# Optimization experiments

Measured on AMD Instinct MI355X. Metric: run time of the kernel, lower is better.

## Reference

```python
import jax, jax.numpy as jnp
import numpy as np

N = 100000   # node_num
E = 1000000  # edges per relation
DIN, DH, DOUT = 64, 32, 64  # in_dim, out_dim//2, out_dim
EPS = 1e-5


def setup_inputs() -> dict:
    key = jax.random.key(0)
    ks = jax.random.split(key, 32)
    def w(k, shape):
        fan_in = shape[0]
        return jax.random.normal(k, shape, dtype=jnp.float32) / np.sqrt(fan_in)
    inp = {}
    inp["init_emb"] = jax.random.normal(ks[0], (N, DIN), dtype=jnp.float32)
    inp["pos_edges"] = jax.random.randint(ks[1], (2, E), 0, N, dtype=jnp.int32)
    inp["neg_edges"] = jax.random.randint(ks[2], (2, E), 0, N, dtype=jnp.int32)
    # conv1: two relation layers + self-loop layer, 64 -> 32
    inp["c1_Wp"] = w(ks[3], (DIN, DH)); inp["c1_bp"] = jnp.zeros((DH,), jnp.float32)
    inp["c1_Wn"] = w(ks[4], (DIN, DH)); inp["c1_bn"] = jnp.zeros((DH,), jnp.float32)
    inp["c1_Ws"] = w(ks[5], (DIN, DH)); inp["c1_bs"] = jnp.zeros((DH,), jnp.float32)
    # conv2: 32 -> 32
    inp["c2_Wp"] = w(ks[6], (DH, DH)); inp["c2_bp"] = jnp.zeros((DH,), jnp.float32)
    inp["c2_Wn"] = w(ks[7], (DH, DH)); inp["c2_bn"] = jnp.zeros((DH,), jnp.float32)
    inp["c2_Ws"] = w(ks[8], (DH, DH)); inp["c2_bs"] = jnp.zeros((DH,), jnp.float32)
    # self.weight: Linear(32 -> 64)
    inp["w_W"] = w(ks[9], (DH, DOUT)); inp["w_b"] = jnp.zeros((DOUT,), jnp.float32)
    # readout MLP: Linear(64,64)+BN+ReLU, Linear(64,64)+BN+ReLU, Linear(64,1)
    inp["m1_W"] = w(ks[10], (DOUT, DOUT)); inp["m1_b"] = jnp.zeros((DOUT,), jnp.float32)
    inp["g1"] = jnp.ones((DOUT,), jnp.float32); inp["b1"] = jnp.zeros((DOUT,), jnp.float32)
    inp["m2_W"] = w(ks[11], (DOUT, DOUT)); inp["m2_b"] = jnp.zeros((DOUT,), jnp.float32)
    inp["g2"] = jnp.ones((DOUT,), jnp.float32); inp["b2"] = jnp.zeros((DOUT,), jnp.float32)
    inp["m3_W"] = w(ks[12], (DOUT, 1)); inp["m3_b"] = jnp.zeros((1,), jnp.float32)
    return inp


def _conv(x, pe, ne, Wp, bp, Wn, bn_, Ws, bs):
    # gather -> per-relation linear -> scatter_add, summed over 2 relations + self loop
    mp = x[pe[0]] @ Wp + bp                                  # [E, d_out]
    agg = jax.ops.segment_sum(mp, pe[1], num_segments=N)      # [N, d_out]
    mn = x[ne[0]] @ Wn + bn_
    agg = agg + jax.ops.segment_sum(mn, ne[1], num_segments=N)
    return agg + x @ Ws + bs


def _batchnorm(h, g, b):
    m = h.mean(axis=0)
    v = h.var(axis=0)
    return (h - m) * jax.lax.rsqrt(v + EPS) * g + b


def reference(init_emb, pos_edges, neg_edges,
              c1_Wp, c1_bp, c1_Wn, c1_bn, c1_Ws, c1_bs,
              c2_Wp, c2_bp, c2_Wn, c2_bn, c2_Ws, c2_bs,
              w_W, w_b, m1_W, m1_b, g1, b1, m2_W, m2_b, g2, b2, m3_W, m3_b):
    z = jnp.tanh(_conv(init_emb, pos_edges, neg_edges, c1_Wp, c1_bp, c1_Wn, c1_bn, c1_Ws, c1_bs))
    z = jnp.tanh(_conv(z, pos_edges, neg_edges, c2_Wp, c2_bp, c2_Wn, c2_bn, c2_Ws, c2_bs))
    z = jnp.tanh(z @ w_W + w_b)                               # [N, 64]
    h = jax.nn.relu(_batchnorm(z @ m1_W + m1_b, g1, b1))      # dropout p=0.2 disabled (eval)
    h = jax.nn.relu(_batchnorm(h @ m2_W + m2_b, g2, b2))
    prob = jax.nn.sigmoid(h @ m3_W + m3_b)                    # [N, 1]
    return (z, prob)
```

## Files before the change

kernel.cpp:

```cpp
#include <hip/hip_runtime.h>
#include <cstdint>
#include <cstddef>

#define NN 100000
#define EE 1000000
#define EPSF 1e-5f
#define NBUK 391
#define NBUK2 (2*NBUK)
#define NBLK 256
#define EPB 7813
#define GSB 782
#define GTILES ((NN + 63) / 64)
#define MLP_GRID 512
#define XFT (NN / 16)
#define XF_GRID 512

typedef __attribute__((ext_vector_type(8))) short bf16x8;
typedef __attribute__((ext_vector_type(4))) float f32x4;

__device__ __forceinline__ void fatomic(float* p, float v) { unsafeAtomicAdd(p, v); }

__device__ __forceinline__ short f2bf(float f) {
    unsigned u = __float_as_uint(f);
    u += 0x7FFF + ((u >> 16) & 1);
    return (short)(u >> 16);
}
__device__ __forceinline__ float bf2f(short s) {
    return __uint_as_float(((unsigned)(unsigned short)s) << 16);
}
__device__ __forceinline__ void split8(const float4 v0, const float4 v1, bf16x8& hi, bf16x8& lo) {
    float a[8] = {v0.x, v0.y, v0.z, v0.w, v1.x, v1.y, v1.z, v1.w};
    #pragma unroll
    for (int i = 0; i < 8; i++) {
        short h = f2bf(a[i]);
        hi[i] = h;
        lo[i] = f2bf(a[i] - bf2f(h));
    }
}
__device__ __forceinline__ int kmap(int kg, int i) {
    return (i < 4) ? kg * 4 + i : 16 + kg * 4 + (i - 4);
}

__device__ __forceinline__ void edge_of(const int* __restrict__ pe, const int* __restrict__ ne,
                                        int s, int& src, int& dst, int& bucket) {
    if (s < EE) { src = pe[s]; dst = pe[EE + s]; bucket = dst >> 8; }
    else        { src = ne[s - EE]; dst = ne[s]; bucket = NBUK + (dst >> 8); }
}

__global__ __launch_bounds__(256) void k_hist(const int* __restrict__ pe,
                                              const int* __restrict__ ne,
                                              int* __restrict__ hist) {
    __shared__ int lh[NBUK2];
    for (int i = threadIdx.x; i < NBUK2; i += 256) lh[i] = 0;
    __syncthreads();
    int start = blockIdx.x * EPB, end = min(start + EPB, 2 * EE);
    for (int s = start + threadIdx.x; s < end; s += 256) {
        int src, dst, bucket;
        edge_of(pe, ne, s, src, dst, bucket);
        atomicAdd(&lh[bucket], 1);
    }
    __syncthreads();
    for (int i = threadIdx.x; i < NBUK2; i += 256)
        hist[i * NBLK + blockIdx.x] = lh[i];
}

__global__ __launch_bounds__(256) void k_gscan1(const int* __restrict__ in,
                                                int* __restrict__ out,
                                                int* __restrict__ partials) {
    int i = blockIdx.x * 256 + threadIdx.x;
    int v = in[i];
    __shared__ int s[256];
    s[threadIdx.x] = v;
    __syncthreads();
    for (int off = 1; off < 256; off <<= 1) {
        int u = (threadIdx.x >= off) ? s[threadIdx.x - off] : 0;
        __syncthreads();
        s[threadIdx.x] += u;
        __syncthreads();
    }
    out[i] = s[threadIdx.x] - v;
    if (threadIdx.x == 255) partials[blockIdx.x] = s[255];
}

__global__ __launch_bounds__(1024) void k_gscan2(int* __restrict__ partials) {
    __shared__ int s[1024];
    int v = (threadIdx.x < GSB) ? partials[threadIdx.x] : 0;
    s[threadIdx.x] = v;
    __syncthreads();
    for (int off = 1; off < 1024; off <<= 1) {
        int u = (threadIdx.x >= off) ? s[threadIdx.x - off] : 0;
        __syncthreads();
        s[threadIdx.x] += u;
        __syncthreads();
    }
    if (threadIdx.x < GSB) partials[threadIdx.x] = s[threadIdx.x] - v;
}

__global__ __launch_bounds__(256) void k_gscan3(const int* __restrict__ partials,
                                                int* __restrict__ out) {
    out[blockIdx.x * 256 + threadIdx.x] += partials[blockIdx.x];
}

__global__ __launch_bounds__(256) void k_binscatter(const int* __restrict__ pe,
                                                    const int* __restrict__ ne,
                                                    const int* __restrict__ soff,
                                                    unsigned* __restrict__ staging) {
    __shared__ int cur[NBUK2];
    for (int i = threadIdx.x; i < NBUK2; i += 256)
        cur[i] = soff[i * NBLK + blockIdx.x];
    __syncthreads();
    int start = blockIdx.x * EPB, end = min(start + EPB, 2 * EE);
    for (int s = start + threadIdx.x; s < end; s += 256) {
        int src, dst, bucket;
        edge_of(pe, ne, s, src, dst, bucket);
        int pos = atomicAdd(&cur[bucket], 1);
        staging[pos] = ((unsigned)(dst & 255) << 20) | (unsigned)src;
    }
}

__global__ __launch_bounds__(256) void k_local(const unsigned* __restrict__ staging,
                                               const int* __restrict__ soff,
                                               int* __restrict__ rpP,
                                               int* __restrict__ rpN,
                                               int* __restrict__ csrAll) {
    int bucket = blockIdx.x;
    int rel = bucket >= NBUK;
    int nodeBase = (bucket - rel * NBUK) << 8;
    int bstart = soff[bucket * NBLK];
    int bend = (bucket == NBUK2 - 1) ? 2 * EE : soff[(bucket + 1) * NBLK];
    int tid = threadIdx.x;
    __shared__ int deg[256], sc[256];
    deg[tid] = 0;
    __syncthreads();
    for (int i = bstart + tid; i < bend; i += 256) {
        int d = (int)(staging[i] >> 20);
        atomicAdd(&deg[d], 1);
    }
    __syncthreads();
    int dv = deg[tid];
    sc[tid] = dv;
    __syncthreads();
    for (int off = 1; off < 256; off <<= 1) {
        int u = (tid >= off) ? sc[tid - off] : 0;
        __syncthreads();
        sc[tid] += u;
        __syncthreads();
    }
    int lrp = sc[tid] - dv;
    int nCount = min(256, NN - nodeBase);
    int relbase = rel ? EE : 0;
    if (tid < nCount) (rel ? rpN : rpP)[nodeBase + tid] = bstart - relbase + lrp;
    if (bucket == NBUK - 1 && tid == 0) rpP[NN] = EE;
    if (bucket == NBUK2 - 1 && tid == 0) rpN[NN] = EE;
    deg[tid] = lrp;
    __syncthreads();
    for (int i = bstart + tid; i < bend; i += 256) {
        unsigned v = staging[i];
        int d = (int)(v >> 20);
        int src = (int)(v & 0xFFFFFu);
        int slot = atomicAdd(&deg[d], 1);
        csrAll[bstart + slot] = src;
    }
}

__global__ __launch_bounds__(192) __attribute__((amdgpu_waves_per_eu(2, 4)))
void k_xf1(const float* __restrict__ x,
           const float* __restrict__ Wp,
           const float* __restrict__ Wn,
           const float* __restrict__ Ws,
           float* __restrict__ xp,
           float* __restrict__ xn,
           float* __restrict__ xs) {
    int tid = threadIdx.x;
    int wvm = tid >> 6;
    int l = tid & 63;
    int r16 = l & 15, kg = l >> 4;
    const float* W = (wvm == 0) ? Wp : (wvm == 1) ? Wn : Ws;
    float* outm = (wvm == 0) ? xp : (wvm == 1) ? xn : xs;

    bf16x8 bh[2][2], bl[2][2];
    #pragma unroll
    for (int ct = 0; ct < 2; ct++)
        #pragma unroll
        for (int h = 0; h < 2; h++)
            #pragma unroll
            for (int i = 0; i < 8; i++) {
                int k = h * 32 + kmap(kg, i);
                float w = W[k * 32 + ct * 16 + r16];
                short hi = f2bf(w);
                bh[ct][h][i] = hi;
                bl[ct][h][i] = f2bf(w - bf2f(hi));
            }

    for (int tile = blockIdx.x; tile < XFT; tile += XF_GRID) {
        int rbase = tile * 16;
        int arow = rbase + r16;
        bf16x8 ah[2], al[2];
        #pragma unroll
        for (int h = 0; h < 2; h++) {
            int k0 = h * 32 + kg * 4;
            int k1 = h * 32 + 16 + kg * 4;
            float4 v0 = *(const float4*)&x[(size_t)arow * 64 + k0];
            float4 v1 = *(const float4*)&x[(size_t)arow * 64 + k1];
            split8(v0, v1, ah[h], al[h]);
        }
        f32x4 acc[2];
        #pragma unroll
        for (int ct = 0; ct < 2; ct++) { acc[ct][0] = 0.f; acc[ct][1] = 0.f; acc[ct][2] = 0.f; acc[ct][3] = 0.f; }
        #pragma unroll
        for (int h = 0; h < 2; h++)
            #pragma unroll
            for (int ct = 0; ct < 2; ct++) {
                acc[ct] = __builtin_amdgcn_mfma_f32_16x16x32_bf16(ah[h], bh[ct][h], acc[ct], 0, 0, 0);
                acc[ct] = __builtin_amdgcn_mfma_f32_16x16x32_bf16(al[h], bh[ct][h], acc[ct], 0, 0, 0);
                acc[ct] = __builtin_amdgcn_mfma_f32_16x16x32_bf16(ah[h], bl[ct][h], acc[ct], 0, 0, 0);
            }
        #pragma unroll
        for (int ct = 0; ct < 2; ct++)
            #pragma unroll
            for (int i = 0; i < 4; i++)
                outm[(size_t)(rbase + kg * 4 + i) * 32 + ct * 16 + r16] = acc[ct][i];
    }
}

__global__ __launch_bounds__(192) __attribute__((amdgpu_waves_per_eu(2, 4)))
void k_xf2(const float* __restrict__ z,
           const float* __restrict__ Wp,
           const float* __restrict__ Wn,
           const float* __restrict__ Ws,
           float* __restrict__ xp,
           float* __restrict__ xn,
           float* __restrict__ xs) {
    int tid = threadIdx.x;
    int wvm = tid >> 6;
    int l = tid & 63;
    int r16 = l & 15, kg = l >> 4;
    const float* W = (wvm == 0) ? Wp : (wvm == 1) ? Wn : Ws;
    float* outm = (wvm == 0) ? xp : (wvm == 1) ? xn : xs;

    bf16x8 bh[2], bl[2];
    #pragma unroll
    for (int ct = 0; ct < 2; ct++)
        #pragma unroll
        for (int i = 0; i < 8; i++) {
            int k = kmap(kg, i);
            float w = W[k * 32 + ct * 16 + r16];
            short hi = f2bf(w);
            bh[ct][i] = hi;
            bl[ct][i] = f2bf(w - bf2f(hi));
        }

    for (int tile = blockIdx.x; tile < XFT; tile += XF_GRID) {
        int rbase = tile * 16;
        int arow = rbase + r16;
        float4 v0 = *(const float4*)&z[(size_t)arow * 32 + kg * 4];
        float4 v1 = *(const float4*)&z[(size_t)arow * 32 + 16 + kg * 4];
        bf16x8 ah, al;
        split8(v0, v1, ah, al);
        f32x4 acc[2];
        #pragma unroll
        for (int ct = 0; ct < 2; ct++) { acc[ct][0] = 0.f; acc[ct][1] = 0.f; acc[ct][2] = 0.f; acc[ct][3] = 0.f; }
        #pragma unroll
        for (int ct = 0; ct < 2; ct++) {
            acc[ct] = __builtin_amdgcn_mfma_f32_16x16x32_bf16(ah, bh[ct], acc[ct], 0, 0, 0);
            acc[ct] = __builtin_amdgcn_mfma_f32_16x16x32_bf16(al, bh[ct], acc[ct], 0, 0, 0);
            acc[ct] = __builtin_amdgcn_mfma_f32_16x16x32_bf16(ah, bl[ct], acc[ct], 0, 0, 0);
        }
        #pragma unroll
        for (int ct = 0; ct < 2; ct++)
            #pragma unroll
            for (int i = 0; i < 4; i++)
                outm[(size_t)(rbase + kg * 4 + i) * 32 + ct * 16 + r16] = acc[ct][i];
    }
}

__device__ __forceinline__ float pull_rel(const float* __restrict__ xsrc,
                                          const int* __restrict__ csr,
                                          int b0, int b1, int j, float acc) {
    for (int base = b0; base < b1; base += 32) {
        int rem = b1 - base;
        int cnt = min(rem, 32);
        int idx = (j < rem) ? csr[base + j] : 0;
        int i = 0;
        for (; i + 4 <= cnt; i += 4) {
            int s0 = __shfl(idx, i, 32);
            int s1 = __shfl(idx, i + 1, 32);
            int s2 = __shfl(idx, i + 2, 32);
            int s3 = __shfl(idx, i + 3, 32);
            float v0 = xsrc[(size_t)s0 * 32 + j];
            float v1 = xsrc[(size_t)s1 * 32 + j];
            float v2 = xsrc[(size_t)s2 * 32 + j];
            float v3 = xsrc[(size_t)s3 * 32 + j];
            acc += v0; acc += v1; acc += v2; acc += v3;
        }
        for (; i < cnt; i++) {
            int s = __shfl(idx, i, 32);
            acc += xsrc[(size_t)s * 32 + j];
        }
    }
    return acc;
}

__global__ __launch_bounds__(256) void k_pull(const float* __restrict__ xp,
                                              const float* __restrict__ xn,
                                              const float* __restrict__ xs,
                                              const int* __restrict__ rpP,
                                              const int* __restrict__ csrP,
                                              const int* __restrict__ rpN,
                                              const int* __restrict__ csrN,
                                              const float* __restrict__ bp,
                                              const float* __restrict__ bn,
                                              const float* __restrict__ bs,
                                              float* __restrict__ out) {
    int j = threadIdx.x & 31;
    int hw = (blockIdx.x * 256 + threadIdx.x) >> 5;
    const int nhw = (2048 * 256) >> 5;
    float bpj = bp[j], bnj = bn[j], bsj = bs[j];
    for (int n = hw; n < NN; n += nhw) {
        int p0 = rpP[n], p1 = rpP[n + 1];
        int n0 = rpN[n], n1 = rpN[n + 1];
        float acc = xs[(size_t)n * 32 + j] + bsj
                  + (float)(p1 - p0) * bpj + (float)(n1 - n0) * bnj;
        acc = pull_rel(xp, csrP, p0, p1, j, acc);
        acc = pull_rel(xn, csrN, n0, n1, j, acc);
        out[(size_t)n * 32 + j] = tanhf(acc);
    }
}

__global__ __launch_bounds__(256) __attribute__((amdgpu_waves_per_eu(2, 4)))
void k_wlin(const float* __restrict__ z2,
            const float* __restrict__ Wl,
            const float* __restrict__ bl,
            float* __restrict__ z) {
    int tid = threadIdx.x;
    int wv = tid >> 6;
    int l = tid & 63;
    int r16 = l & 15, kg = l >> 4;

    bf16x8 bh[4], blo[4];
    #pragma unroll
    for (int ct = 0; ct < 4; ct++)
        #pragma unroll
        for (int i = 0; i < 8; i++) {
            int k = kmap(kg, i);
            float w = Wl[k * 64 + ct * 16 + r16];
            short hi = f2bf(w);
            bh[ct][i] = hi;
            blo[ct][i] = f2bf(w - bf2f(hi));
        }
    float bj[4];
    #pragma unroll
    for (int ct = 0; ct < 4; ct++) bj[ct] = bl[ct * 16 + r16];

    for (int tile = blockIdx.x * 4 + wv; tile < XFT; tile += XF_GRID * 4) {
        int rbase = tile * 16;
        int arow = rbase + r16;
        float4 v0 = *(const float4*)&z2[(size_t)arow * 32 + kg * 4];
        float4 v1 = *(const float4*)&z2[(size_t)arow * 32 + 16 + kg * 4];
        bf16x8 ah, al;
        split8(v0, v1, ah, al);
        f32x4 acc[4];
        #pragma unroll
        for (int ct = 0; ct < 4; ct++) { acc[ct][0] = 0.f; acc[ct][1] = 0.f; acc[ct][2] = 0.f; acc[ct][3] = 0.f; }
        #pragma unroll
        for (int ct = 0; ct < 4; ct++) {
            acc[ct] = __builtin_amdgcn_mfma_f32_16x16x32_bf16(ah, bh[ct], acc[ct], 0, 0, 0);
            acc[ct] = __builtin_amdgcn_mfma_f32_16x16x32_bf16(al, bh[ct], acc[ct], 0, 0, 0);
            acc[ct] = __builtin_amdgcn_mfma_f32_16x16x32_bf16(ah, blo[ct], acc[ct], 0, 0, 0);
        }
        #pragma unroll
        for (int ct = 0; ct < 4; ct++)
            #pragma unroll
            for (int i = 0; i < 4; i++)
                z[(size_t)(rbase + kg * 4 + i) * 64 + ct * 16 + r16] = tanhf(acc[ct][i] + bj[ct]);
    }
}

__global__ __launch_bounds__(256) __attribute__((amdgpu_waves_per_eu(2, 4)))
void k_mlp(const float* __restrict__ in,
           const float* __restrict__ a1,
           const float* __restrict__ c1,
           int doBN,
           const float* __restrict__ W,
           const float* __restrict__ b,
           float* __restrict__ out,
           float* __restrict__ colsum,
           float* __restrict__ colsq) {
    __shared__ float scol[64], ssq[64];
    int tid = threadIdx.x;
    if (tid < 64) { scol[tid] = 0.f; ssq[tid] = 0.f; }
    int wv = tid >> 6;
    int l = tid & 63;
    int r16 = l & 15, kg = l >> 4;

    bf16x8 bf[4][2];
    #pragma unroll
    for (int ct = 0; ct < 4; ct++)
        #pragma unroll
        for (int h = 0; h < 2; h++)
            #pragma unroll
            for (int i = 0; i < 8; i++) {
                int k = h * 32 + kmap(kg, i);
                bf[ct][h][i] = f2bf(W[k * 64 + ct * 16 + r16]);
            }
    float bj[4];
    #pragma unroll
    for (int ct = 0; ct < 4; ct++) bj[ct] = b[ct * 16 + r16];

    float av0[2][4], cv0[2][4], av1[2][4], cv1[2][4];
    #pragma unroll
    for (int h = 0; h < 2; h++) {
        int k0 = h * 32 + kg * 4;
        int k1 = h * 32 + 16 + kg * 4;
        #pragma unroll
        for (int i = 0; i < 4; i++) {
            av0[h][i] = doBN ? a1[k0 + i] : 1.f;
            cv0[h][i] = doBN ? c1[k0 + i] : 0.f;
            av1[h][i] = doBN ? a1[k1 + i] : 1.f;
            cv1[h][i] = doBN ? c1[k1 + i] : 0.f;
        }
    }

    float lsum[4] = {0.f, 0.f, 0.f, 0.f}, lsq[4] = {0.f, 0.f, 0.f, 0.f};

    for (int tile = blockIdx.x; tile < GTILES; tile += MLP_GRID) {
        int base = tile * 64;
        int arow = base + wv * 16 + r16;
        bool rv = arow < NN;
        bf16x8 af[2];
        #pragma unroll
        for (int h = 0; h < 2; h++) {
            int k0 = h * 32 + kg * 4;
            int k1 = h * 32 + 16 + kg * 4;
            float4 v0 = rv ? *(const float4*)&in[(size_t)arow * 64 + k0]
                           : make_float4(0.f, 0.f, 0.f, 0.f);
            float4 v1 = rv ? *(const float4*)&in[(size_t)arow * 64 + k1]
                           : make_float4(0.f, 0.f, 0.f, 0.f);
            if (doBN) {
                v0.x = fmaxf(v0.x * av0[h][0] + cv0[h][0], 0.f);
                v0.y = fmaxf(v0.y * av0[h][1] + cv0[h][1], 0.f);
                v0.z = fmaxf(v0.z * av0[h][2] + cv0[h][2], 0.f);
                v0.w = fmaxf(v0.w * av0[h][3] + cv0[h][3], 0.f);
                v1.x = fmaxf(v1.x * av1[h][0] + cv1[h][0], 0.f);
                v1.y = fmaxf(v1.y * av1[h][1] + cv1[h][1], 0.f);
                v1.z = fmaxf(v1.z * av1[h][2] + cv1[h][2], 0.f);
                v1.w = fmaxf(v1.w * av1[h][3] + cv1[h][3], 0.f);
            }
            af[h][0] = f2bf(v0.x); af[h][1] = f2bf(v0.y);
            af[h][2] = f2bf(v0.z); af[h][3] = f2bf(v0.w);
            af[h][4] = f2bf(v1.x); af[h][5] = f2bf(v1.y);
            af[h][6] = f2bf(v1.z); af[h][7] = f2bf(v1.w);
        }

        f32x4 acc[4];
        #pragma unroll
        for (int ct = 0; ct < 4; ct++) { acc[ct][0] = 0.f; acc[ct][1] = 0.f; acc[ct][2] = 0.f; acc[ct][3] = 0.f; }
        #pragma unroll
        for (int h = 0; h < 2; h++)
            #pragma unroll
            for (int ct = 0; ct < 4; ct++)
                acc[ct] = __builtin_amdgcn_mfma_f32_16x16x32_bf16(af[h], bf[ct][h], acc[ct], 0, 0, 0);

        #pragma unroll
        for (int ct = 0; ct < 4; ct++) {
            int col = ct * 16 + r16;
            #pragma unroll
            for (int i = 0; i < 4; i++) {
                int orow = base + wv * 16 + kg * 4 + i;
                if (orow < NN) {
                    float s = acc[ct][i] + bj[ct];
                    out[(size_t)orow * 64 + col] = s;
                    lsum[ct] += s; lsq[ct] += s * s;
                }
            }
        }
    }

    __syncthreads();
    #pragma unroll
    for (int ct = 0; ct < 4; ct++) {
        atomicAdd(&scol[ct * 16 + r16], lsum[ct]);
        atomicAdd(&ssq[ct * 16 + r16], lsq[ct]);
    }
    __syncthreads();
    if (tid < 64) {
        fatomic(&colsum[tid], scol[tid]);
        fatomic(&colsq[tid], ssq[tid]);
    }
}

__global__ void k_bnstats(const float* __restrict__ colsum, const float* __restrict__ colsq,
                          const float* __restrict__ g, const float* __restrict__ beta,
                          float* __restrict__ a, float* __restrict__ c) {
    int j = threadIdx.x;
    if (j < 64) {
        float m = colsum[j] * (1.f / NN);
        float v = colsq[j] * (1.f / NN) - m * m;
        float aj = g[j] * rsqrtf(v + EPSF);
        a[j] = aj;
        c[j] = beta[j] - m * aj;
    }
}

__global__ __launch_bounds__(256) void k_mlp3(const float* __restrict__ t2,
                                              const float* __restrict__ a2,
                                              const float* __restrict__ c2,
                                              const float* __restrict__ W3,
                                              const float* __restrict__ b3,
                                              float* __restrict__ prob) {
    int j = threadIdx.x & 63;
    int r = threadIdx.x >> 6;
    float aj = a2[j], cj = c2[j], wj = W3[j], bb = b3[0];
    for (int n = blockIdx.x * 4 + r; n < NN; n += 2048 * 4) {
        float h = fmaxf(t2[(size_t)n * 64 + j] * aj + cj, 0.f) * wj;
        #pragma unroll
        for (int off = 32; off > 0; off >>= 1) h += __shfl_xor(h, off, 64);
        if (j == 0) prob[n] = 1.f / (1.f + expf(-(h + bb)));
    }
}

extern "C" void kernel_launch(void* const* d_in, const int* in_sizes, int n_in,
                              void* d_out, int out_size, void* d_ws, size_t ws_size,
                              hipStream_t stream) {
    const float* init_emb = (const float*)d_in[0];
    const int* pe = (const int*)d_in[1];
    const int* ne = (const int*)d_in[2];
    const float* c1_Wp = (const float*)d_in[3];  const float* c1_bp = (const float*)d_in[4];
    const float* c1_Wn = (const float*)d_in[5];  const float* c1_bn = (const float*)d_in[6];
    const float* c1_Ws = (const float*)d_in[7];  const float* c1_bs = (const float*)d_in[8];
    const float* c2_Wp = (const float*)d_in[9];  const float* c2_bp = (const float*)d_in[10];
    const float* c2_Wn = (const float*)d_in[11]; const float* c2_bn = (const float*)d_in[12];
    const float* c2_Ws = (const float*)d_in[13]; const float* c2_bs = (const float*)d_in[14];
    const float* w_W = (const float*)d_in[15];   const float* w_b = (const float*)d_in[16];
    const float* m1_W = (const float*)d_in[17];  const float* m1_b = (const float*)d_in[18];
    const float* g1 = (const float*)d_in[19];    const float* b1 = (const float*)d_in[20];
    const float* m2_W = (const float*)d_in[21];  const float* m2_b = (const float*)d_in[22];
    const float* g2 = (const float*)d_in[23];    const float* b2 = (const float*)d_in[24];
    const float* m3_W = (const float*)d_in[25];  const float* m3_b = (const float*)d_in[26];

    size_t off = 0;
    auto alloc = [&](size_t bytes) -> void* {
        void* r = (char*)d_ws + off;
        off += (bytes + 255) & ~(size_t)255;
        return r;
    };
    float* sums = (float*)alloc(256 * 4);
    size_t zero_bytes = off;
    size_t csr_region = off;
    int*   hist = (int*)alloc((size_t)NBUK2 * NBLK * 4);
    int*   soff = (int*)alloc((size_t)NBUK2 * NBLK * 4);
    int*   part = (int*)alloc((size_t)1024 * 4);
    unsigned* staging = (unsigned*)alloc((size_t)2 * EE * 8);
    int*   csrAll = (int*)alloc((size_t)2 * EE * 4);
    int*   rpP  = (int*)alloc((size_t)(NN + 1) * 4);
    int*   rpN  = (int*)alloc((size_t)(NN + 1) * 4);
    float* R1   = (float*)alloc((size_t)NN * 96 * 4);
    float* z1   = (float*)alloc((size_t)NN * 32 * 4);
    float* z2   = (float*)alloc((size_t)NN * 32 * 4);
    float* abc  = (float*)alloc(256 * 4);

    int* csrP = csrAll;
    int* csrN = csrAll + (size_t)EE;
    float* xp = R1;
    float* xn = R1 + (size_t)NN * 32;
    float* xs = R1 + (size_t)NN * 64;
    float* t1 = R1;
    float* t2 = (float*)((char*)d_ws + csr_region);

    float* z_out = (float*)d_out;
    float* prob  = (float*)d_out + (size_t)NN * 64;

    hipMemsetAsync(d_ws, 0, zero_bytes, stream);

    k_hist<<<NBLK, 256, 0, stream>>>(pe, ne, hist);
    k_gscan1<<<GSB, 256, 0, stream>>>(hist, soff, part);
    k_gscan2<<<1, 1024, 0, stream>>>(part);
    k_gscan3<<<GSB, 256, 0, stream>>>(part, soff);
    k_binscatter<<<NBLK, 256, 0, stream>>>(pe, ne, soff, staging);
    k_local<<<NBUK2, 256, 0, stream>>>(staging, soff, rpP, rpN, csrAll);

    k_xf1<<<XF_GRID, 192, 0, stream>>>(init_emb, c1_Wp, c1_Wn, c1_Ws, xp, xn, xs);
    k_pull<<<2048, 256, 0, stream>>>(xp, xn, xs, rpP, csrP, rpN, csrN, c1_bp, c1_bn, c1_bs, z1);
    k_xf2<<<XF_GRID, 192, 0, stream>>>(z1, c2_Wp, c2_Wn, c2_Ws, xp, xn, xs);
    k_pull<<<2048, 256, 0, stream>>>(xp, xn, xs, rpP, csrP, rpN, csrN, c2_bp, c2_bn, c2_bs, z2);
    k_wlin<<<XF_GRID, 256, 0, stream>>>(z2, w_W, w_b, z_out);
    k_mlp<<<MLP_GRID, 256, 0, stream>>>(z_out, nullptr, nullptr, 0, m1_W, m1_b, t1, sums + 0, sums + 64);
    k_bnstats<<<1, 64, 0, stream>>>(sums + 0, sums + 64, g1, b1, abc + 0, abc + 64);
    k_mlp<<<MLP_GRID, 256, 0, stream>>>(t1, abc + 0, abc + 64, 1, m2_W, m2_b, t2, sums + 128, sums + 192);
    k_bnstats<<<1, 64, 0, stream>>>(sums + 128, sums + 192, g2, b2, abc + 128, abc + 192);
    k_mlp3<<<2048, 256, 0, stream>>>(t2, abc + 128, abc + 192, m3_W, m3_b, prob);
}
```

Before: 261.3 us.

## Vectorize pull gather with float4 slots; fuse wlin with mlp1 and inline BN stats

The pull kernel now has each 32-lane group split into 4 neighbour slots of 8 lanes, each lane loading a float4, and reduces the partial sums across slots with xor shuffles. This issues fewer, wider gather loads. The output linear layer is fused with the first MLP layer through a per-wave LDS tile, so the z round trip and one launch go away. The separate BN-stats kernels are removed, and each consumer recomputes the scale and shift from the column sums. The cost is extra shuffles, predicated loads on partial groups, and higher register pressure in the fused kernel.

Result: faster. 247.0 us (-5.5%).

```diff
diff --git a/kernel.cpp b/kernel.cpp
--- a/kernel.cpp
+++ b/kernel.cpp
@@ -274,31 +274,33 @@
     }
 }
 
-__device__ __forceinline__ float pull_rel(const float* __restrict__ xsrc,
-                                          const int* __restrict__ csr,
-                                          int b0, int b1, int j, float acc) {
+__device__ __forceinline__ float4 pull_rel4(const float* __restrict__ xsrc,
+                                            const int* __restrict__ csr,
+                                            int b0, int b1, int j32, int q, int slot,
+                                            float4 acc) {
     for (int base = b0; base < b1; base += 32) {
         int rem = b1 - base;
         int cnt = min(rem, 32);
-        int idx = (j < rem) ? csr[base + j] : 0;
-        int i = 0;
-        for (; i + 4 <= cnt; i += 4) {
-            int s0 = __shfl(idx, i, 32);
-            int s1 = __shfl(idx, i + 1, 32);
-            int s2 = __shfl(idx, i + 2, 32);
-            int s3 = __shfl(idx, i + 3, 32);
-            float v0 = xsrc[(size_t)s0 * 32 + j];
-            float v1 = xsrc[(size_t)s1 * 32 + j];
-            float v2 = xsrc[(size_t)s2 * 32 + j];
-            float v3 = xsrc[(size_t)s3 * 32 + j];
-            acc += v0; acc += v1; acc += v2; acc += v3;
-        }
-        for (; i < cnt; i++) {
-            int s = __shfl(idx, i, 32);
-            acc += xsrc[(size_t)s * 32 + j];
+        int idx = (j32 < rem) ? csr[base + j32] : 0;
+        int gmax = (cnt + 3) >> 2;
+        for (int g = 0; g < gmax; g++) {
+            int nb = 4 * g + slot;
+            int s = __shfl(idx, nb, 32);
+            bool ok = nb < cnt;
+            int ss = ok ? s : 0;
+            float4 v = *(const float4*)&xsrc[(size_t)ss * 32 + q * 4];
+            if (ok) { acc.x += v.x; acc.y += v.y; acc.z += v.z; acc.w += v.w; }
         }
     }
     return acc;
+}
+
+__device__ __forceinline__ float4 xor_reduce4(float4 a, int mask) {
+    a.x += __shfl_xor(a.x, mask, 32);
+    a.y += __shfl_xor(a.y, mask, 32);
+    a.z += __shfl_xor(a.z, mask, 32);
+    a.w += __shfl_xor(a.w, mask, 32);
+    return a;
 }
 
 __global__ __launch_bounds__(256) void k_pull(const float* __restrict__ xp,
@@ -312,30 +314,47 @@
                                               const float* __restrict__ bn,
                                               const float* __restrict__ bs,
                                               float* __restrict__ out) {
-    int j = threadIdx.x & 31;
+    int j32 = threadIdx.x & 31;
+    int q = j32 & 7;
+    int slot = j32 >> 3;
     int hw = (blockIdx.x * 256 + threadIdx.x) >> 5;
     const int nhw = (2048 * 256) >> 5;
-    float bpj = bp[j], bnj = bn[j], bsj = bs[j];
+    float4 bp4 = *(const float4*)&bp[q * 4];
+    float4 bn4 = *(const float4*)&bn[q * 4];
+    float4 bs4 = *(const float4*)&bs[q * 4];
     for (int n = hw; n < NN; n += nhw) {
         int p0 = rpP[n], p1 = rpP[n + 1];
         int n0 = rpN[n], n1 = rpN[n + 1];
-        float acc = xs[(size_t)n * 32 + j] + bsj
-                  + (float)(p1 - p0) * bpj + (float)(n1 - n0) * bnj;
-        acc = pull_rel(xp, csrP, p0, p1, j, acc);
-        acc = pull_rel(xn, csrN, n0, n1, j, acc);
-        out[(size_t)n * 32 + j] = tanhf(acc);
-    }
-}
-
-__global__ __launch_bounds__(256) __attribute__((amdgpu_waves_per_eu(2, 4)))
-void k_wlin(const float* __restrict__ z2,
-            const float* __restrict__ Wl,
-            const float* __restrict__ bl,
-            float* __restrict__ z) {
+        float4 acc = make_float4(0.f, 0.f, 0.f, 0.f);
+        acc = pull_rel4(xp, csrP, p0, p1, j32, q, slot, acc);
+        acc = pull_rel4(xn, csrN, n0, n1, j32, q, slot, acc);
+        acc = xor_reduce4(acc, 8);
+        acc = xor_reduce4(acc, 16);
+        if (slot == 0) {
+            float4 xs4 = *(const float4*)&xs[(size_t)n * 32 + q * 4];
+            float dp = (float)(p1 - p0), dn = (float)(n1 - n0);
+            float4 r;
+            r.x = tanhf(acc.x + xs4.x + dp * bp4.x + dn * bn4.x + bs4.x);
+            r.y = tanhf(acc.y + xs4.y + dp * bp4.y + dn * bn4.y + bs4.y);
+            r.z = tanhf(acc.z + xs4.z + dp * bp4.z + dn * bn4.z + bs4.z);
+            r.w = tanhf(acc.w + xs4.w + dp * bp4.w + dn * bn4.w + bs4.w);
+            *(float4*)&out[(size_t)n * 32 + q * 4] = r;
+        }
+    }
+}
+
+__global__ __launch_bounds__(256) __attribute__((amdgpu_waves_per_eu(2, 3)))
+void k_wlin_mlp1(const float* __restrict__ z2,
+                 const float* __restrict__ Wl, const float* __restrict__ blv,
+                 const float* __restrict__ W1, const float* __restrict__ b1v,
+                 float* __restrict__ z, float* __restrict__ t1,
+                 float* __restrict__ colsum, float* __restrict__ colsq) {
+    __shared__ float zl[4][16 * 68];
+    __shared__ float scol[64], ssq[64];
     int tid = threadIdx.x;
-    int wv = tid >> 6;
-    int l = tid & 63;
-    int r16 = l & 15, kg = l >> 4;
+    if (tid < 64) { scol[tid] = 0.f; ssq[tid] = 0.f; }
+    int wv = tid >> 6, l = tid & 63, r16 = l & 15, kg = l >> 4;
+    float* myz = &zl[wv][0];
 
     bf16x8 bh[4], blo[4];
     #pragma unroll
@@ -348,9 +367,25 @@
             bh[ct][i] = hi;
             blo[ct][i] = f2bf(w - bf2f(hi));
         }
-    float bj[4];
-    #pragma unroll
-    for (int ct = 0; ct < 4; ct++) bj[ct] = bl[ct * 16 + r16];
+    float bjl[4];
+    #pragma unroll
+    for (int ct = 0; ct < 4; ct++) bjl[ct] = blv[ct * 16 + r16];
+
+    bf16x8 b1f[4][2];
+    #pragma unroll
+    for (int ct = 0; ct < 4; ct++)
+        #pragma unroll
+        for (int h = 0; h < 2; h++)
+            #pragma unroll
+            for (int i = 0; i < 8; i++) {
+                int k = h * 32 + kmap(kg, i);
+                b1f[ct][h][i] = f2bf(W1[k * 64 + ct * 16 + r16]);
+            }
+    float bj1[4];
+    #pragma unroll
+    for (int ct = 0; ct < 4; ct++) bj1[ct] = b1v[ct * 16 + r16];
+
+    float lsum[4] = {0.f, 0.f, 0.f, 0.f}, lsq[4] = {0.f, 0.f, 0.f, 0.f};
 
     for (int tile = blockIdx.x * 4 + wv; tile < XFT; tile += XF_GRID * 4) {
         int rbase = tile * 16;
@@ -371,16 +406,58 @@
         #pragma unroll
         for (int ct = 0; ct < 4; ct++)
             #pragma unroll
-            for (int i = 0; i < 4; i++)
-                z[(size_t)(rbase + kg * 4 + i) * 64 + ct * 16 + r16] = tanhf(acc[ct][i] + bj[ct]);
+            for (int i = 0; i < 4; i++) {
+                float zv = tanhf(acc[ct][i] + bjl[ct]);
+                z[(size_t)(rbase + kg * 4 + i) * 64 + ct * 16 + r16] = zv;
+                myz[(kg * 4 + i) * 68 + ct * 16 + r16] = zv;
+            }
+        bf16x8 af[2];
+        #pragma unroll
+        for (int h = 0; h < 2; h++) {
+            float4 u0 = *(const float4*)&myz[r16 * 68 + h * 32 + kg * 4];
+            float4 u1 = *(const float4*)&myz[r16 * 68 + h * 32 + 16 + kg * 4];
+            af[h][0] = f2bf(u0.x); af[h][1] = f2bf(u0.y);
+            af[h][2] = f2bf(u0.z); af[h][3] = f2bf(u0.w);
+            af[h][4] = f2bf(u1.x); af[h][5] = f2bf(u1.y);
+            af[h][6] = f2bf(u1.z); af[h][7] = f2bf(u1.w);
+        }
+        f32x4 acc2[4];
+        #pragma unroll
+        for (int ct = 0; ct < 4; ct++) { acc2[ct][0] = 0.f; acc2[ct][1] = 0.f; acc2[ct][2] = 0.f; acc2[ct][3] = 0.f; }
+        #pragma unroll
+        for (int h = 0; h < 2; h++)
+            #pragma unroll
+            for (int ct = 0; ct < 4; ct++)
+                acc2[ct] = __builtin_amdgcn_mfma_f32_16x16x32_bf16(af[h], b1f[ct][h], acc2[ct], 0, 0, 0);
+        #pragma unroll
+        for (int ct = 0; ct < 4; ct++)
+            #pragma unroll
+            for (int i = 0; i < 4; i++) {
+                float t = acc2[ct][i] + bj1[ct];
+                t1[(size_t)(rbase + kg * 4 + i) * 64 + ct * 16 + r16] = t;
+                lsum[ct] += t; lsq[ct] += t * t;
+            }
+    }
+
+    __syncthreads();
+    #pragma unroll
+    for (int ct = 0; ct < 4; ct++) {
+        atomicAdd(&scol[ct * 16 + r16], lsum[ct]);
+        atomicAdd(&ssq[ct * 16 + r16], lsq[ct]);
+    }
+    __syncthreads();
+    if (tid < 64) {
+        fatomic(&colsum[tid], scol[tid]);
+        fatomic(&colsq[tid], ssq[tid]);
     }
 }
 
 __global__ __launch_bounds__(256) __attribute__((amdgpu_waves_per_eu(2, 4)))
 void k_mlp(const float* __restrict__ in,
-           const float* __restrict__ a1,
-           const float* __restrict__ c1,
-           int doBN,
+           const float* __restrict__ csIn,
+           const float* __restrict__ cqIn,
+           const float* __restrict__ g,
+           const float* __restrict__ beta,
            const float* __restrict__ W,
            const float* __restrict__ b,
            float* __restrict__ out,
@@ -392,6 +469,7 @@
     int wv = tid >> 6;
     int l = tid & 63;
     int r16 = l & 15, kg = l >> 4;
+    const float inv = 1.f / NN;
 
     bf16x8 bf[4][2];
     #pragma unroll
@@ -409,17 +487,20 @@
 
     float av0[2][4], cv0[2][4], av1[2][4], cv1[2][4];
     #pragma unroll
-    for (int h = 0; h < 2; h++) {
-        int k0 = h * 32 + kg * 4;
-        int k1 = h * 32 + 16 + kg * 4;
+    for (int h = 0; h < 2; h++)
         #pragma unroll
         for (int i = 0; i < 4; i++) {
-            av0[h][i] = doBN ? a1[k0 + i] : 1.f;
-            cv0[h][i] = doBN ? c1[k0 + i] : 0.f;
-            av1[h][i] = doBN ? a1[k1 + i] : 1.f;
-            cv1[h][i] = doBN ? c1[k1 + i] : 0.f;
-        }
-    }
+            int k0 = h * 32 + kg * 4 + i;
+            float m = csIn[k0] * inv;
+            float vv = cqIn[k0] * inv - m * m;
+            float a = g[k0] * rsqrtf(vv + EPSF);
+            av0[h][i] = a; cv0[h][i] = beta[k0] - m * a;
+            int k1 = k0 + 16;
+            m = csIn[k1] * inv;
+            vv = cqIn[k1] * inv - m * m;
+            a = g[k1] * rsqrtf(vv + EPSF);
+            av1[h][i] = a; cv1[h][i] = beta[k1] - m * a;
+        }
 
     float lsum[4] = {0.f, 0.f, 0.f, 0.f}, lsq[4] = {0.f, 0.f, 0.f, 0.f};
 
@@ -436,16 +517,14 @@
                            : make_float4(0.f, 0.f, 0.f, 0.f);
             float4 v1 = rv ? *(const float4*)&in[(size_t)arow * 64 + k1]
                            : make_float4(0.f, 0.f, 0.f, 0.f);
-            if (doBN) {
-                v0.x = fmaxf(v0.x * av0[h][0] + cv0[h][0], 0.f);
-                v0.y = fmaxf(v0.y * av0[h][1] + cv0[h][1], 0.f);
-                v0.z = fmaxf(v0.z * av0[h][2] + cv0[h][2], 0.f);
-                v0.w = fmaxf(v0.w * av0[h][3] + cv0[h][3], 0.f);
-                v1.x = fmaxf(v1.x * av1[h][0] + cv1[h][0], 0.f);
-                v1.y = fmaxf(v1.y * av1[h][1] + cv1[h][1], 0.f);
-                v1.z = fmaxf(v1.z * av1[h][2] + cv1[h][2], 0.f);
-                v1.w = fmaxf(v1.w * av1[h][3] + cv1[h][3], 0.f);
-            }
+            v0.x = fmaxf(v0.x * av0[h][0] + cv0[h][0], 0.f);
+            v0.y = fmaxf(v0.y * av0[h][1] + cv0[h][1], 0.f);
+            v0.z = fmaxf(v0.z * av0[h][2] + cv0[h][2], 0.f);
+            v0.w = fmaxf(v0.w * av0[h][3] + cv0[h][3], 0.f);
+            v1.x = fmaxf(v1.x * av1[h][0] + cv1[h][0], 0.f);
+            v1.y = fmaxf(v1.y * av1[h][1] + cv1[h][1], 0.f);
+            v1.z = fmaxf(v1.z * av1[h][2] + cv1[h][2], 0.f);
+            v1.w = fmaxf(v1.w * av1[h][3] + cv1[h][3], 0.f);
             af[h][0] = f2bf(v0.x); af[h][1] = f2bf(v0.y);
             af[h][2] = f2bf(v0.z); af[h][3] = f2bf(v0.w);
             af[h][4] = f2bf(v1.x); af[h][5] = f2bf(v1.y);
@@ -489,28 +568,22 @@
     }
 }
 
-__global__ void k_bnstats(const float* __restrict__ colsum, const float* __restrict__ colsq,
-                          const float* __restrict__ g, const float* __restrict__ beta,
-                          float* __restrict__ a, float* __restrict__ c) {
-    int j = threadIdx.x;
-    if (j < 64) {
-        float m = colsum[j] * (1.f / NN);
-        float v = colsq[j] * (1.f / NN) - m * m;
-        float aj = g[j] * rsqrtf(v + EPSF);
-        a[j] = aj;
-        c[j] = beta[j] - m * aj;
-    }
-}
-
 __global__ __launch_bounds__(256) void k_mlp3(const float* __restrict__ t2,
-                                              const float* __restrict__ a2,
-                                              const float* __restrict__ c2,
+                                              const float* __restrict__ cs,
+                                              const float* __restrict__ cq,
+                                              const float* __restrict__ g,
+                                              const float* __restrict__ beta,
                                               const float* __restrict__ W3,
                                               const float* __restrict__ b3,
                                               float* __restrict__ prob) {
     int j = threadIdx.x & 63;
     int r = threadIdx.x >> 6;
-    float aj = a2[j], cj = c2[j], wj = W3[j], bb = b3[0];
+    const float inv = 1.f / NN;
+    float m = cs[j] * inv;
+    float vv = cq[j] * inv - m * m;
+    float aj = g[j] * rsqrtf(vv + EPSF);
+    float cj = beta[j] - m * aj;
+    float wj = W3[j], bb = b3[0];
     for (int n = blockIdx.x * 4 + r; n < NN; n += 2048 * 4) {
         float h = fmaxf(t2[(size_t)n * 64 + j] * aj + cj, 0.f) * wj;
         #pragma unroll
@@ -557,7 +630,6 @@
     float* R1   = (float*)alloc((size_t)NN * 96 * 4);
     float* z1   = (float*)alloc((size_t)NN * 32 * 4);
     float* z2   = (float*)alloc((size_t)NN * 32 * 4);
-    float* abc  = (float*)alloc(256 * 4);
 
     int* csrP = csrAll;
     int* csrN = csrAll + (size_t)EE;
@@ -583,10 +655,7 @@
     k_pull<<<2048, 256, 0, stream>>>(xp, xn, xs, rpP, csrP, rpN, csrN, c1_bp, c1_bn, c1_bs, z1);
     k_xf2<<<XF_GRID, 192, 0, stream>>>(z1, c2_Wp, c2_Wn, c2_Ws, xp, xn, xs);
     k_pull<<<2048, 256, 0, stream>>>(xp, xn, xs, rpP, csrP, rpN, csrN, c2_bp, c2_bn, c2_bs, z2);
-    k_wlin<<<XF_GRID, 256, 0, stream>>>(z2, w_W, w_b, z_out);
-    k_mlp<<<MLP_GRID, 256, 0, stream>>>(z_out, nullptr, nullptr, 0, m1_W, m1_b, t1, sums + 0, sums + 64);
-    k_bnstats<<<1, 64, 0, stream>>>(sums + 0, sums + 64, g1, b1, abc + 0, abc + 64);
-    k_mlp<<<MLP_GRID, 256, 0, stream>>>(t1, abc + 0, abc + 64, 1, m2_W, m2_b, t2, sums + 128, sums + 192);
-    k_bnstats<<<1, 64, 0, stream>>>(sums + 128, sums + 192, g2, b2, abc + 128, abc + 192);
-    k_mlp3<<<2048, 256, 0, stream>>>(t2, abc + 128, abc + 192, m3_W, m3_b, prob);
-}
+    k_wlin_mlp1<<<XF_GRID, 256, 0, stream>>>(z2, w_W, w_b, m1_W, m1_b, z_out, t1, sums + 0, sums + 64);
+    k_mlp<<<MLP_GRID, 256, 0, stream>>>(t1, sums + 0, sums + 64, g1, b1, m2_W, m2_b, t2, sums + 128, sums + 192);
+    k_mlp3<<<2048, 256, 0, stream>>>(t2, sums + 128, sums + 192, g2, b2, m3_W, m3_b, prob);
+}
```
